# Performance work log

Measured on AMD Instinct MI355X. Metric: run time of the kernel, lower is better.

## Reference

```python
import jax, jax.numpy as jnp
import numpy as np

IMAGE_SIZE = 256
DET = int(IMAGE_SIZE * 2 ** 0.5 + 0.5)  # 362 detector bins (diagonal coverage)
US = 4
N_ACQ = 45                     # acquired views: 0,4,...,176 degrees
N_FULL = (N_ACQ - 1) * US + 1  # 177 full (upsampled) views


def setup_inputs() -> dict:
    key = jax.random.key(0)
    k1, k2 = jax.random.split(key)
    x_source = jax.random.normal(k1, (2, 1, IMAGE_SIZE, IMAGE_SIZE), jnp.float32)
    s_target = jax.random.normal(k2, (2, 1, DET, N_ACQ), jnp.float32)
    theta_acq = np.arange(0, 180, 4, dtype=np.float64)  # 45 acquired angles
    segs = [np.linspace(theta_acq[i], theta_acq[i + 1], US + 1)[:-1] for i in range(N_ACQ - 1)]
    theta_full = np.concatenate(segs + [theta_acq[-1:]]).astype(np.float32)  # [177]
    acq_idx = (np.arange(N_ACQ) * US).astype(np.int32)  # positions of acquired angles in theta_full
    return {"x_source": x_source, "s_target": s_target,
            "thetas_deg": jnp.asarray(theta_full), "acq_idx": jnp.asarray(acq_idx)}


def bilinear_gather(img, xs, ys):
    # img: [B,C,H,W]; xs, ys: pixel coords [A,det,det]; zero outside the image.
    H, W = img.shape[-2], img.shape[-1]
    x0 = jnp.floor(xs); y0 = jnp.floor(ys)
    wx = xs - x0; wy = ys - y0
    x0i = x0.astype(jnp.int32); y0i = y0.astype(jnp.int32)

    def get(yi, xi):
        valid = (xi >= 0) & (xi < W) & (yi >= 0) & (yi < H)
        v = img[:, :, jnp.clip(yi, 0, H - 1), jnp.clip(xi, 0, W - 1)]  # [B,C,A,det,det]
        return jnp.where(valid, v, 0.0)

    return (get(y0i, x0i) * (1 - wy) * (1 - wx)
            + get(y0i, x0i + 1) * (1 - wy) * wx
            + get(y0i + 1, x0i) * wy * (1 - wx)
            + get(y0i + 1, x0i + 1) * wy * wx)


def radon(x, thetas_rad, det):
    # Ray-sum projection: sino[theta, t] = sum_s image(t*cos - s*sin, t*sin + s*cos)
    B, C, H, W = x.shape
    t = jnp.arange(det, dtype=x.dtype) - (det - 1) / 2.0  # centered detector/ray coord
    cos = jnp.cos(thetas_rad)[:, None, None]
    sin = jnp.sin(thetas_rad)[:, None, None]
    T = t[None, :, None]; S = t[None, None, :]
    xs = T * cos - S * sin + (W - 1) / 2.0  # [A,det,det]
    ys = T * sin + S * cos + (H - 1) / 2.0
    return bilinear_gather(x, xs, ys).sum(-1)  # [B,C,A,det]


def ramp_filter(size):
    # skimage/pytorch_radon style ramp built from its real-space kernel
    n = np.concatenate([np.arange(1, size // 2 + 1, 2), np.arange(size // 2 - 1, 0, -2)])
    f = np.zeros(size)
    f[0] = 0.25
    f[1::2] = -1.0 / (np.pi * n) ** 2
    return jnp.asarray(2 * np.real(np.fft.fft(f)), dtype=jnp.float32)


def fbp(sino, thetas_rad, image_size):
    # Filtered back-projection. sino: [B,C,det,A]
    B, C, det, A = sino.shape
    pad = max(64, int(2 ** np.ceil(np.log2(2 * det))))
    filt = ramp_filter(pad)  # [pad]
    sp = jnp.pad(sino, ((0, 0), (0, 0), (0, pad - det), (0, 0)))
    sf = jnp.fft.ifft(jnp.fft.fft(sp, axis=2) * filt[None, None, :, None], axis=2).real
    sf = jnp.transpose(sf[:, :, :det, :], (0, 1, 3, 2)).astype(sino.dtype)  # [B,C,A,det]
    g = jnp.arange(image_size, dtype=sino.dtype) - (image_size - 1) / 2.0
    cos = jnp.cos(thetas_rad); sin = jnp.sin(thetas_rad)
    # detector coordinate hit by each pixel, per angle: t = x*cos + y*sin
    t = (cos[:, None, None] * g[None, None, :]
         + sin[:, None, None] * g[None, :, None] + (det - 1) / 2.0)  # [A,H,W]
    t = t.reshape(A, -1)
    t0 = jnp.floor(t)
    w = t - t0
    t0i = t0.astype(jnp.int32)
    aidx = jnp.arange(A)[:, None]

    def samp(ti):
        valid = (ti >= 0) & (ti < det)
        return jnp.where(valid, sf[:, :, aidx, jnp.clip(ti, 0, det - 1)], 0.0)  # [B,C,A,HW]

    v = samp(t0i) * (1 - w) + samp(t0i + 1) * w
    reco = v.sum(2) * (jnp.pi / (2 * A))
    return reco.reshape(B, C, image_size, image_size)


def reference(x_source, s_target, thetas_deg, acq_idx):
    th = thetas_deg * (jnp.pi / 180.0)
    s = radon(x_source, th, DET)          # [B,C,A,det]
    s = jnp.transpose(s, (0, 1, 3, 2))    # [B,C,det,A] -- angle axis last, as in the module
    # masked data-consistency update: acquired columns become (target - predicted)
    s = s.at[..., acq_idx].set(s_target - s[..., acq_idx])
    return fbp(s, th, IMAGE_SIZE)
```

## Files before the change

### kernel.cpp

```cpp
#include <hip/hip_runtime.h>
#include <math.h>

#define IMG   256
#define NFULL 177
#define DETN  362
#define NACQ  45
#define PAD   1024

#define SINO_OFF 0
#define SF_OFF   131072

#define HALF_T 180.5f
#define SEGL   32
#define TILE_W 1664

__constant__ const int kStripOrd[46] =
    {22,23,21,24,20,25,19,26,18,27,17,28,16,29,15,30,14,31,13,32,
     12,33,11,34,10,35,9,36,8,37,7,38,6,39,5,40,4,41,3,42,2,43,1,44,0,45};

__device__ __forceinline__ void gload16(const float* g, float* l) {
    __builtin_amdgcn_global_load_lds(
        (const __attribute__((address_space(1))) void*)g,
        (__attribute__((address_space(3))) void*)l, 16, 0, 0);
}

template<int P>
__device__ __forceinline__ float radon_strip(
    const float* __restrict__ img,
    float* tb,
    const float c, const float s,
    const float xbase, const float ybase,
    const float xAB_mn, const float yAB_mn, const float yAB_mx,
    const int Slo, const int Shi, const int lane)
{
    constexpr int W4   = P / 4;
    constexpr int HMAX = TILE_W / P;
    const int ts = lane & 7;
    float val = 0.0f;

    for (int Sseg = Slo; Sseg < Shi; Sseg += SEGL) {
        const float sv0 = (float)Sseg - HALF_T;
        const float sv1 = sv0 + (float)(SEGL - 1);
        const float xmn = xAB_mn - sv1 * s;
        const float ya  = sv0 * c, yb = sv1 * c;
        const float ymn = yAB_mn + fminf(ya, yb);
        const float ymx = yAB_mx + fmaxf(ya, yb);
        const int ix0  = (int)floorf(xmn) - 1;
        const int iy0  = (int)floorf(ymn) - 1;
        const int ix0a = ix0 & ~3;
        const int h    = min((int)floorf(ymx) + 3 - iy0, HMAX);
        const int total4 = W4 * h;
        const int nfull  = total4 & ~63;
        const bool interior = (ix0a >= 0) & (iy0 >= 0) &
                              (ix0a + P <= IMG) & (iy0 + h <= IMG);

        asm volatile("s_waitcnt lgkmcnt(0)" ::: "memory");

        if (interior) {
            const float* __restrict__ src = img + iy0 * IMG + ix0a;
            for (int f0 = 0; f0 < nfull; f0 += 64) {
                const int f  = f0 + lane;
                const int r  = f / W4;
                const int c4 = f - r * W4;
                gload16(src + r * IMG + (c4 << 2), tb + (f0 << 2));
            }
            const int f = nfull + lane;
            if (f < total4) {
                const int r  = f / W4;
                const int c4 = f - r * W4;
                gload16(src + r * IMG + (c4 << 2), tb + (nfull << 2));
            }
        } else {
            for (int f = lane; f < total4; f += 64) {
                const int r  = f / W4;
                const int c4 = f - r * W4;
                const int gy = iy0 + r;
                const int gx = ix0a + (c4 << 2);
                const bool ok = ((unsigned)gy < (unsigned)IMG) &
                                ((unsigned)gx <= (unsigned)(IMG - 4));
                float4 v = make_float4(0.f, 0.f, 0.f, 0.f);
                if (ok) v = *(const float4*)(img + gy * IMG + gx);
                *(float4*)(tb + (f << 2)) = v;
            }
        }
        asm volatile("s_waitcnt vmcnt(0) lgkmcnt(0)" ::: "memory");
        __builtin_amdgcn_sched_barrier(0);

        const float xoff = xbase - (float)ix0a;
        const float yoff = ybase - (float)iy0;
        const int Send = min(Sseg + SEGL, Shi);

        auto samp = [&](float sval) {
            const float xs  = fmaf(-sval, s, xoff);
            const float ys  = fmaf(sval, c, yoff);
            const float x0f = floorf(xs);
            const float y0f = floorf(ys);
            const float wx  = xs - x0f;
            const float wy  = ys - y0f;
            const int base = (int)fmaf(y0f, (float)P, x0f);
            const float v00 = tb[base];
            const float v01 = tb[base + 1];
            const float v10 = tb[base + P];
            const float v11 = tb[base + P + 1];
            const float h0 = fmaf(wx, v01 - v00, v00);
            const float h1 = fmaf(wx, v11 - v10, v10);
            val += fmaf(wy, h1 - h0, h0);
        };

        if (Send - Sseg == SEGL) {
            const float s0 = (float)(Sseg + ts) - HALF_T;
            #pragma unroll
            for (int u = 0; u < SEGL / 8; ++u) samp(s0 + (float)(8 * u));
        } else {
            for (int S = Sseg + ts; S < Send; S += 8) samp((float)S - HALF_T);
        }
    }
    return val;
}

__global__ __launch_bounds__(64, 6) void radon_kernel(
    const float* __restrict__ x,
    const float* __restrict__ thetas,
    float* __restrict__ sino)
{
    const int blk = blockIdx.x;
    const int b = blk / NFULL;
    const int a = blk - b * NFULL;
    const int lane = threadIdx.x & 63;
    const int sp   = kStripOrd[blockIdx.y];
    const int T0   = sp << 3;
    const int tt   = lane >> 3;
    const int ts   = lane & 7;
    const int T    = T0 + tt;

    __shared__ __align__(16) float tile[TILE_W];

    const float th = thetas[a] * (float)(M_PI / 180.0);
    const float c = cosf(th);
    const float s = sinf(th);
    const float cx = (IMG - 1) * 0.5f;
    const float cy = (IMG - 1) * 0.5f;
    const float Tc = (float)T - HALF_T;
    const float xbase = Tc * c + cx;
    const float ybase = Tc * s + cy;

    float lo = -1e30f, hi = 1e30f;
    bool empty = (T >= DETN);
    {   const float aa = -s;
        if (aa > 1e-5f)       { lo = fmaxf(lo, (-1.0f - xbase) / aa); hi = fminf(hi, (256.0f - xbase) / aa); }
        else if (aa < -1e-5f) { lo = fmaxf(lo, (256.0f - xbase) / aa); hi = fminf(hi, (-1.0f - xbase) / aa); }
        else if (xbase <= -1.0f || xbase >= 256.0f) empty = true;
    }
    {   const float aa = c;
        if (aa > 1e-5f)       { lo = fmaxf(lo, (-1.0f - ybase) / aa); hi = fminf(hi, (256.0f - ybase) / aa); }
        else if (aa < -1e-5f) { lo = fmaxf(lo, (256.0f - ybase) / aa); hi = fminf(hi, (-1.0f - ybase) / aa); }
        else if (ybase <= -1.0f || ybase >= 256.0f) empty = true;
    }
    lo = fmaxf(lo, -200.0f);
    hi = fminf(hi, 200.0f);
    int Slo = max(0, (int)floorf(lo + HALF_T) - 1);
    int Shi = min(DETN, (int)floorf(hi + HALF_T) + 2);
    if (empty || Shi < Slo) { Slo = 0; Shi = 0; }

    int wlo = (Shi > Slo) ? Slo : DETN;
    int whi = (Shi > Slo) ? Shi : 0;
    #pragma unroll
    for (int d = 1; d < 64; d <<= 1) {
        wlo = min(wlo, __shfl_xor(wlo, d, 64));
        whi = max(whi, __shfl_xor(whi, d, 64));
    }

    int best = 2;
    {
        const float ac = fabsf(c), as = fabsf(s);
        const float spanx = 7.f * ac + 31.f * as;
        const float spany = 7.f * as + 31.f * ac;
        const float Pc[6] = {36.f, 40.f, 44.f, 48.f, 52.f, 56.f};
        const int   Hm[6] = {46, 41, 37, 34, 32, 29};
        int bcost = 1 << 30;
        #pragma unroll
        for (int p = 0; p < 6; ++p) {
            const float Pf = Pc[p];
            const float dT = s * Pf + c;
            const float dS = c * Pf - s;
            const int bank = (int)floorf((float)tt * dT + (float)ts * dS + 0.5f) & 31;
            unsigned long long m = ~0ull;
            #pragma unroll
            for (int bit = 0; bit < 5; ++bit) {
                const unsigned long long bb = __ballot((bank >> bit) & 1);
                m &= ((bank >> bit) & 1) ? bb : ~bb;
            }
            int cnt = __popcll(m);
            #pragma unroll
            for (int d = 1; d < 64; d <<= 1) cnt = max(cnt, __shfl_xor(cnt, d, 64));
            const bool fit = (spanx <= Pf - 8.05f) && (spany <= (float)Hm[p] - 5.05f);
            if (fit && cnt < bcost) { bcost = cnt; best = p; }
        }
    }

    const float TcA = (float)T0 - HALF_T;
    const float TcB = (float)(T0 + 7) - HALF_T;
    const float xAB_mn = fminf(TcA * c + cx, TcB * c + cx);
    const float yAB_mn = fminf(TcA * s + cy, TcB * s + cy);
    const float yAB_mx = fmaxf(TcA * s + cy, TcB * s + cy);

    const float* __restrict__ img = x + b * IMG * IMG;

    float val;
    switch (best) {
    case 0:  val = radon_strip<36>(img, tile, c, s, xbase, ybase,
                                   xAB_mn, yAB_mn, yAB_mx, wlo, whi, lane); break;
    case 1:  val = radon_strip<40>(img, tile, c, s, xbase, ybase,
                                   xAB_mn, yAB_mn, yAB_mx, wlo, whi, lane); break;
    case 2:  val = radon_strip<44>(img, tile, c, s, xbase, ybase,
                                   xAB_mn, yAB_mn, yAB_mx, wlo, whi, lane); break;
    case 3:  val = radon_strip<48>(img, tile, c, s, xbase, ybase,
                                   xAB_mn, yAB_mn, yAB_mx, wlo, whi, lane); break;
    case 4:  val = radon_strip<52>(img, tile, c, s, xbase, ybase,
                                   xAB_mn, yAB_mn, yAB_mx, wlo, whi, lane); break;
    default: val = radon_strip<56>(img, tile, c, s, xbase, ybase,
                                   xAB_mn, yAB_mn, yAB_mx, wlo, whi, lane); break;
    }

    val += __shfl_xor(val, 1, 8);
    val += __shfl_xor(val, 2, 8);
    val += __shfl_xor(val, 4, 8);
    if (ts == 0 && T < DETN) {
        sino[(b * NFULL + a) * DETN + T] = val;
    }
}

__global__ __launch_bounds__(192) void dc_filter_kernel(
    const float* __restrict__ sino,
    const float* __restrict__ st,
    const int*   __restrict__ acq,
    float* __restrict__ sf)
{
    const int blk = blockIdx.x;
    const int b = blk / NFULL;
    const int a = blk - b * NFULL;
    const int tid = threadIdx.x;

    __shared__ float col[DETN];
    __shared__ float gf[PAD];

    const float SC = (float)(M_PI / (2.0 * NFULL));
    const float c0 = 0.5f * SC;
    for (int n = tid; n < PAD; n += 192) {
        float v = 0.0f;
        if (n & 1) {
            const int d = (n < PAD - n) ? n : (PAD - n);
            const float pd = (float)M_PI * (float)d;
            v = -2.0f / (pd * pd) * SC;
        }
        gf[n] = v;
    }

    int inv = -1;
    for (int i = 0; i < NACQ; ++i) {
        if (acq[i] == a) inv = i;
    }

    for (int m = tid; m < DETN; m += 192) {
        float val = sino[(b * NFULL + a) * DETN + m];
        if (inv >= 0) {
            val = st[(b * DETN + m) * NACQ + inv] - val;
        }
        col[m] = val;
    }
    __syncthreads();

    const int T = blockIdx.y * 181 + tid;
    if (tid < 181) {
        const int m0 = (T + 1) & 1;
        float acc = c0 * col[T];
        #pragma unroll 4
        for (int k = 0; k < 181; ++k) {
            const int m = m0 + 2 * k;
            acc += col[m] * gf[(T - m) & (PAD - 1)];
        }
        sf[(b * NFULL + a) * DETN + T] = acc;
    }
}

__global__ __launch_bounds__(256) void backproject_kernel(
    const float* __restrict__ sf,
    const float* __restrict__ thetas,
    float* __restrict__ out)
{
    __shared__ float cb[2 * NFULL];
    __shared__ float red[256];
    const int tid = threadIdx.x;
    const int lane  = tid & 63;
    const int phase = tid >> 6;
    const int pix = blockIdx.x * 64 + lane;
    const int b = pix >> 16;
    const int y = (pix >> 8) & 255;
    const int xq = pix & 255;
    const float gx = (float)xq - (IMG - 1) * 0.5f;
    const float gy = (float)y  - (IMG - 1) * 0.5f;

    for (int a = tid; a < NFULL; a += 256) {
        float th = thetas[a] * (float)(M_PI / 180.0);
        cb[2 * a]     = cosf(th);
        cb[2 * a + 1] = fmaf(sinf(th), gy, HALF_T);
    }
    __syncthreads();

    const float* __restrict__ sfb = sf + b * NFULL * DETN;

    float acc = 0.0f;
    #pragma unroll 4
    for (int a = phase; a < NFULL; a += 4) {
        const float cs = cb[2 * a];
        const float bs = cb[2 * a + 1];
        const float t = fmaf(cs, gx, bs);
        const float t0f = floorf(t);
        const float w = t - t0f;
        const float* row = sfb + a * DETN + (int)t0f;
        const float v0 = row[0];
        const float v1 = row[1];
        acc += v0 + w * (v1 - v0);
    }
    red[tid] = acc;
    __syncthreads();
    if (tid < 64) {
        out[blockIdx.x * 64 + tid] =
            red[tid] + red[tid + 64] + red[tid + 128] + red[tid + 192];
    }
}

extern "C" void kernel_launch(void* const* d_in, const int* in_sizes, int n_in,
                              void* d_out, int out_size, void* d_ws, size_t ws_size,
                              hipStream_t stream) {
    const float* x      = (const float*)d_in[0];
    const float* st     = (const float*)d_in[1];
    const float* thetas = (const float*)d_in[2];
    const int*   acq    = (const int*)d_in[3];
    float* out  = (float*)d_out;
    float* wsf  = (float*)d_ws;
    float* sino = wsf + SINO_OFF;
    float* sf   = wsf + SF_OFF;

    dim3 gA(2 * NFULL, 46);
    radon_kernel<<<gA, 64, 0, stream>>>(x, thetas, sino);
    dim3 gB(2 * NFULL, 2);
    dc_filter_kernel<<<gB, 192, 0, stream>>>(sino, st, acq, sf);
    backproject_kernel<<<(2 * IMG * IMG) / 64, 256, 0, stream>>>(sf, thetas, out);
}
```

Before: 124.9 us.

## Process both batch images per radon block to share geometry and sampling math

Each radon block now handles both batch images for one angle and detector strip. Both image tiles are staged into a doubled LDS buffer, and one set of sample coordinates and weights drives the interpolation for both. This halves the grid and removes the duplicated per-block setup: the trig, ray clipping, the bank-conflict-driven pitch selection, and the address math. In exchange, each block uses twice the LDS and more registers, the occupancy hint drops from 6 to 4, and there are fewer blocks to hide latency.

```diff
diff --git a/kernel.cpp b/kernel.cpp
--- a/kernel.cpp
+++ b/kernel.cpp
@@ -25,8 +25,9 @@
 }
 
 template<int P>
-__device__ __forceinline__ float radon_strip(
-    const float* __restrict__ img,
+__device__ __forceinline__ float2 radon_strip2(
+    const float* __restrict__ img0,
+    const float* __restrict__ img1,
     float* tb,
     const float c, const float s,
     const float xbase, const float ybase,
@@ -36,7 +37,7 @@
     constexpr int W4   = P / 4;
     constexpr int HMAX = TILE_W / P;
     const int ts = lane & 7;
-    float val = 0.0f;
+    float val0 = 0.0f, val1 = 0.0f;
 
     for (int Sseg = Slo; Sseg < Shi; Sseg += SEGL) {
         const float sv0 = (float)Sseg - HALF_T;
@@ -57,18 +58,22 @@
         asm volatile("s_waitcnt lgkmcnt(0)" ::: "memory");
 
         if (interior) {
-            const float* __restrict__ src = img + iy0 * IMG + ix0a;
+            const int base0 = iy0 * IMG + ix0a;
             for (int f0 = 0; f0 < nfull; f0 += 64) {
                 const int f  = f0 + lane;
                 const int r  = f / W4;
                 const int c4 = f - r * W4;
-                gload16(src + r * IMG + (c4 << 2), tb + (f0 << 2));
+                const int go = base0 + r * IMG + (c4 << 2);
+                gload16(img0 + go, tb + (f0 << 2));
+                gload16(img1 + go, tb + TILE_W + (f0 << 2));
             }
             const int f = nfull + lane;
             if (f < total4) {
                 const int r  = f / W4;
                 const int c4 = f - r * W4;
-                gload16(src + r * IMG + (c4 << 2), tb + (nfull << 2));
+                const int go = base0 + r * IMG + (c4 << 2);
+                gload16(img0 + go, tb + (nfull << 2));
+                gload16(img1 + go, tb + TILE_W + (nfull << 2));
             }
         } else {
             for (int f = lane; f < total4; f += 64) {
@@ -78,9 +83,15 @@
                 const int gx = ix0a + (c4 << 2);
                 const bool ok = ((unsigned)gy < (unsigned)IMG) &
                                 ((unsigned)gx <= (unsigned)(IMG - 4));
-                float4 v = make_float4(0.f, 0.f, 0.f, 0.f);
-                if (ok) v = *(const float4*)(img + gy * IMG + gx);
-                *(float4*)(tb + (f << 2)) = v;
+                float4 v0 = make_float4(0.f, 0.f, 0.f, 0.f);
+                float4 v1 = v0;
+                if (ok) {
+                    const int go = gy * IMG + gx;
+                    v0 = *(const float4*)(img0 + go);
+                    v1 = *(const float4*)(img1 + go);
+                }
+                *(float4*)(tb + (f << 2)) = v0;
+                *(float4*)(tb + TILE_W + (f << 2)) = v1;
             }
         }
         asm volatile("s_waitcnt vmcnt(0) lgkmcnt(0)" ::: "memory");
@@ -98,13 +109,20 @@
             const float wx  = xs - x0f;
             const float wy  = ys - y0f;
             const int base = (int)fmaf(y0f, (float)P, x0f);
-            const float v00 = tb[base];
-            const float v01 = tb[base + 1];
-            const float v10 = tb[base + P];
-            const float v11 = tb[base + P + 1];
-            const float h0 = fmaf(wx, v01 - v00, v00);
-            const float h1 = fmaf(wx, v11 - v10, v10);
-            val += fmaf(wy, h1 - h0, h0);
+            const float a00 = tb[base];
+            const float a01 = tb[base + 1];
+            const float a10 = tb[base + P];
+            const float a11 = tb[base + P + 1];
+            const float b00 = tb[TILE_W + base];
+            const float b01 = tb[TILE_W + base + 1];
+            const float b10 = tb[TILE_W + base + P];
+            const float b11 = tb[TILE_W + base + P + 1];
+            const float ah0 = fmaf(wx, a01 - a00, a00);
+            const float ah1 = fmaf(wx, a11 - a10, a10);
+            val0 += fmaf(wy, ah1 - ah0, ah0);
+            const float bh0 = fmaf(wx, b01 - b00, b00);
+            const float bh1 = fmaf(wx, b11 - b10, b10);
+            val1 += fmaf(wy, bh1 - bh0, bh0);
         };
 
         if (Send - Sseg == SEGL) {
@@ -115,17 +133,15 @@
             for (int S = Sseg + ts; S < Send; S += 8) samp((float)S - HALF_T);
         }
     }
-    return val;
-}
-
-__global__ __launch_bounds__(64, 6) void radon_kernel(
+    return make_float2(val0, val1);
+}
+
+__global__ __launch_bounds__(64, 4) void radon_kernel(
     const float* __restrict__ x,
     const float* __restrict__ thetas,
     float* __restrict__ sino)
 {
-    const int blk = blockIdx.x;
-    const int b = blk / NFULL;
-    const int a = blk - b * NFULL;
+    const int a = blockIdx.x;
     const int lane = threadIdx.x & 63;
     const int sp   = kStripOrd[blockIdx.y];
     const int T0   = sp << 3;
@@ -133,7 +149,7 @@
     const int ts   = lane & 7;
     const int T    = T0 + tt;
 
-    __shared__ __align__(16) float tile[TILE_W];
+    __shared__ __align__(16) float tile[2 * TILE_W];
 
     const float th = thetas[a] * (float)(M_PI / 180.0);
     const float c = cosf(th);
@@ -204,29 +220,34 @@
     const float yAB_mn = fminf(TcA * s + cy, TcB * s + cy);
     const float yAB_mx = fmaxf(TcA * s + cy, TcB * s + cy);
 
-    const float* __restrict__ img = x + b * IMG * IMG;
-
-    float val;
+    const float* __restrict__ img0 = x;
+    const float* __restrict__ img1 = x + IMG * IMG;
+
+    float2 val;
     switch (best) {
-    case 0:  val = radon_strip<36>(img, tile, c, s, xbase, ybase,
-                                   xAB_mn, yAB_mn, yAB_mx, wlo, whi, lane); break;
-    case 1:  val = radon_strip<40>(img, tile, c, s, xbase, ybase,
-                                   xAB_mn, yAB_mn, yAB_mx, wlo, whi, lane); break;
-    case 2:  val = radon_strip<44>(img, tile, c, s, xbase, ybase,
-                                   xAB_mn, yAB_mn, yAB_mx, wlo, whi, lane); break;
-    case 3:  val = radon_strip<48>(img, tile, c, s, xbase, ybase,
-                                   xAB_mn, yAB_mn, yAB_mx, wlo, whi, lane); break;
-    case 4:  val = radon_strip<52>(img, tile, c, s, xbase, ybase,
-                                   xAB_mn, yAB_mn, yAB_mx, wlo, whi, lane); break;
-    default: val = radon_strip<56>(img, tile, c, s, xbase, ybase,
-                                   xAB_mn, yAB_mn, yAB_mx, wlo, whi, lane); break;
-    }
-
-    val += __shfl_xor(val, 1, 8);
-    val += __shfl_xor(val, 2, 8);
-    val += __shfl_xor(val, 4, 8);
+    case 0:  val = radon_strip2<36>(img0, img1, tile, c, s, xbase, ybase,
+                                    xAB_mn, yAB_mn, yAB_mx, wlo, whi, lane); break;
+    case 1:  val = radon_strip2<40>(img0, img1, tile, c, s, xbase, ybase,
+                                    xAB_mn, yAB_mn, yAB_mx, wlo, whi, lane); break;
+    case 2:  val = radon_strip2<44>(img0, img1, tile, c, s, xbase, ybase,
+                                    xAB_mn, yAB_mn, yAB_mx, wlo, whi, lane); break;
+    case 3:  val = radon_strip2<48>(img0, img1, tile, c, s, xbase, ybase,
+                                    xAB_mn, yAB_mn, yAB_mx, wlo, whi, lane); break;
+    case 4:  val = radon_strip2<52>(img0, img1, tile, c, s, xbase, ybase,
+                                    xAB_mn, yAB_mn, yAB_mx, wlo, whi, lane); break;
+    default: val = radon_strip2<56>(img0, img1, tile, c, s, xbase, ybase,
+                                    xAB_mn, yAB_mn, yAB_mx, wlo, whi, lane); break;
+    }
+
+    val.x += __shfl_xor(val.x, 1, 8);
+    val.x += __shfl_xor(val.x, 2, 8);
+    val.x += __shfl_xor(val.x, 4, 8);
+    val.y += __shfl_xor(val.y, 1, 8);
+    val.y += __shfl_xor(val.y, 2, 8);
+    val.y += __shfl_xor(val.y, 4, 8);
     if (ts == 0 && T < DETN) {
-        sino[(b * NFULL + a) * DETN + T] = val;
+        sino[a * DETN + T] = val.x;
+        sino[(NFULL + a) * DETN + T] = val.y;
     }
 }
 
@@ -342,7 +363,7 @@
     float* sino = wsf + SINO_OFF;
     float* sf   = wsf + SF_OFF;
 
-    dim3 gA(2 * NFULL, 46);
+    dim3 gA(NFULL, 46);
     radon_kernel<<<gA, 64, 0, stream>>>(x, thetas, sino);
     dim3 gB(2 * NFULL, 2);
     dc_filter_kernel<<<gB, 192, 0, stream>>>(sino, st, acq, sf);
```

Result: no change. 123.5 us (-1.1%).
